# Performance work log

Measured on AMD Instinct MI355X. Metric: run time of the kernel, lower is better.

## Reference

```python
import jax, jax.numpy as jnp
import numpy as np

T, B, E, H = 512, 128, 512, 512
MEM, CTX = 500, 300

def setup_inputs() -> dict:
    key = jax.random.key(0)
    ks = jax.random.split(key, 16)
    s = 0.05
    return {
        "input_seqs": jax.random.normal(ks[0], (B, T, E), jnp.float32),
        "input_lengths": jax.random.randint(ks[1], (B,), 1, T + 1),
        "Wih_f": jax.random.normal(ks[2], (4 * H, E + CTX), jnp.float32) * s,
        "Whh_f": jax.random.normal(ks[3], (4 * H, H), jnp.float32) * s,
        "bih_f": jax.random.normal(ks[4], (4 * H,), jnp.float32) * s,
        "bhh_f": jax.random.normal(ks[5], (4 * H,), jnp.float32) * s,
        "Wih_b": jax.random.normal(ks[6], (4 * H, E + CTX), jnp.float32) * s,
        "Whh_b": jax.random.normal(ks[7], (4 * H, H), jnp.float32) * s,
        "bih_b": jax.random.normal(ks[8], (4 * H,), jnp.float32) * s,
        "bhh_b": jax.random.normal(ks[9], (4 * H,), jnp.float32) * s,
        "Mk_f": jax.random.normal(ks[10], (MEM, H), jnp.float32) * s,
        "Mv_f": jax.random.normal(ks[11], (CTX, MEM), jnp.float32) * s,
        "Mk_b": jax.random.normal(ks[12], (MEM, H), jnp.float32) * s,
        "Mv_b": jax.random.normal(ks[13], (CTX, MEM), jnp.float32) * s,
    }

def _mem_ctx(h, Mk, Mv):
    # exp-key softmax read: exp(h Mk^T) normalized by row sum, then project to CTX
    a = jnp.exp(h @ Mk.T)                      # [B, MEM]
    return (a / jnp.sum(a, axis=-1, keepdims=True)) @ Mv.T  # [B, CTX]

def _cell(x, h, c, Wih, Whh, b):
    g = x @ Wih.T + h @ Whh.T + b              # [B, 4H], gate order i,f,g,o
    i, f, gg, o = jnp.split(g, 4, axis=-1)
    c = jax.nn.sigmoid(f) * c + jax.nn.sigmoid(i) * jnp.tanh(gg)
    return jax.nn.sigmoid(o) * jnp.tanh(c), c

def reference(input_seqs, input_lengths, Wih_f, Whh_f, bih_f, bhh_f,
              Wih_b, Whh_b, bih_b, bhh_b, Mk_f, Mv_f, Mk_b, Mv_b):
    xs = jnp.transpose(input_seqs, (1, 0, 2))          # [T, B, E]
    dt = xs.dtype
    mask = (jnp.arange(T)[:, None] < input_lengths[None, :]).astype(dt)[:, :, None]  # [T,B,1]
    b_f = bih_f + bhh_f
    b_b = bih_b + bhh_b
    z = jnp.zeros((B, H), dt)
    zf = jnp.zeros((), dt)
    one = jnp.ones((), dt)

    def fstep(carry, x):
        h, c, flag = carry
        ctx = flag * _mem_ctx(h, Mk_f, Mv_f)           # step 0 uses zero dummy context
        h, c = _cell(jnp.concatenate([x, ctx], -1), h, c, Wih_f, Whh_f, b_f)
        return (h, c, one), h
    _, f_hs = jax.lax.scan(fstep, (z, z, zf), xs)      # [T, B, H] per-step hidden

    def bstep(carry, xm):
        x, m = xm
        hm, h, c, flag = carry
        ctx = flag * _mem_ctx(hm, Mk_b, Mv_b)
        h, c = _cell(jnp.concatenate([x, ctx], -1), h, c, Wih_b, Whh_b, b_b)
        return (h * m, h, c, one), None                # masked hidden feeds next memory read
    (h_b, _, _, _), _ = jax.lax.scan(bstep, (z, z, z, zf), (xs[::-1], mask[::-1]))

    idx = jnp.clip(input_lengths - 1, 0, T - 1)
    h_f = f_hs[idx, jnp.arange(B)]                     # final valid forward hidden per example
    # permute(1,2,0).view(B,-1): interleave fwd/bwd per hidden unit
    return jnp.stack([h_f, h_b], axis=-1).reshape(B, 2 * H)
```

## Files before the change

### kernel.cpp

```cpp
#include <hip/hip_runtime.h>
#include <hip/hip_bf16.h>

#define T_   512
#define B_   128
#define E_   512
#define H_   512
#define G4_  2048
#define MEM_ 500
#define CTX_ 300
#define EC_  (E_ + CTX_)

typedef short sh8  __attribute__((ext_vector_type(8)));
typedef float f32x4 __attribute__((ext_vector_type(4)));

struct ScanParams {
  const float* __restrict__ x;
  const short* __restrict__ xbf;
  const int*   __restrict__ len;
  const float* __restrict__ Wih0; const float* __restrict__ Whh0;
  const float* __restrict__ bih0; const float* __restrict__ bhh0;
  const float* __restrict__ Wih1; const float* __restrict__ Whh1;
  const float* __restrict__ bih1; const float* __restrict__ bhh1;
  const float* __restrict__ Mk0;  const float* __restrict__ Mk1;
  const float* __restrict__ Mf;
  short* __restrict__ hbf;
  short* __restrict__ hmbf;
  short* __restrict__ aB;
  unsigned* __restrict__ bar;
  float* __restrict__ out;
};

__device__ __forceinline__ float sigm_(float x) { return 1.f / (1.f + __expf(-x)); }
__device__ __forceinline__ float tanh_(float x) { return 1.f - 2.f / (__expf(2.f * x) + 1.f); }
__device__ __forceinline__ short f2bs(float f) {
  __hip_bfloat16 h = __float2bfloat16(f);
  short s; __builtin_memcpy(&s, &h, 2); return s;
}
__device__ __forceinline__ float bs2f(short s) {
  unsigned u = ((unsigned)(unsigned short)s) << 16;
  float f; __builtin_memcpy(&f, &u, 4); return f;
}

struct F16 { sh8 v[16]; };
__device__ __forceinline__ void gld16(F16& f, const short* base) {
  asm volatile(
      "global_load_dwordx4 %0, %16, off sc0 sc1\n\t"
      "global_load_dwordx4 %1, %16, off offset:64 sc0 sc1\n\t"
      "global_load_dwordx4 %2, %16, off offset:128 sc0 sc1\n\t"
      "global_load_dwordx4 %3, %16, off offset:192 sc0 sc1\n\t"
      "global_load_dwordx4 %4, %16, off offset:256 sc0 sc1\n\t"
      "global_load_dwordx4 %5, %16, off offset:320 sc0 sc1\n\t"
      "global_load_dwordx4 %6, %16, off offset:384 sc0 sc1\n\t"
      "global_load_dwordx4 %7, %16, off offset:448 sc0 sc1\n\t"
      "global_load_dwordx4 %8, %16, off offset:512 sc0 sc1\n\t"
      "global_load_dwordx4 %9, %16, off offset:576 sc0 sc1\n\t"
      "global_load_dwordx4 %10, %16, off offset:640 sc0 sc1\n\t"
      "global_load_dwordx4 %11, %16, off offset:704 sc0 sc1\n\t"
      "global_load_dwordx4 %12, %16, off offset:768 sc0 sc1\n\t"
      "global_load_dwordx4 %13, %16, off offset:832 sc0 sc1\n\t"
      "global_load_dwordx4 %14, %16, off offset:896 sc0 sc1\n\t"
      "global_load_dwordx4 %15, %16, off offset:960 sc0 sc1\n\t"
      "s_waitcnt vmcnt(0)"
      : "=&v"(f.v[0]), "=&v"(f.v[1]), "=&v"(f.v[2]), "=&v"(f.v[3]),
        "=&v"(f.v[4]), "=&v"(f.v[5]), "=&v"(f.v[6]), "=&v"(f.v[7]),
        "=&v"(f.v[8]), "=&v"(f.v[9]), "=&v"(f.v[10]), "=&v"(f.v[11]),
        "=&v"(f.v[12]), "=&v"(f.v[13]), "=&v"(f.v[14]), "=&v"(f.v[15])
      : "v"(base)
      : "memory");
}

__device__ __forceinline__ void st4s(short* base, unsigned d0, unsigned d1,
                                     unsigned d2, unsigned d3) {
  asm volatile(
      "global_store_short %4, %0, off sc0 sc1\n\t"
      "global_store_short %4, %1, off offset:1024 sc0 sc1\n\t"
      "global_store_short %4, %2, off offset:2048 sc0 sc1\n\t"
      "global_store_short %4, %3, off offset:3072 sc0 sc1\n\t"
      "s_waitcnt vmcnt(0)"
      :: "v"(d0), "v"(d1), "v"(d2), "v"(d3), "v"(base) : "memory");
}

__device__ __forceinline__ void st8s(short* base, const unsigned* d) {
  asm volatile(
      "global_store_short %8, %0, off sc0 sc1\n\t"
      "global_store_short %8, %1, off offset:1024 sc0 sc1\n\t"
      "global_store_short %8, %2, off offset:2048 sc0 sc1\n\t"
      "global_store_short %8, %3, off offset:3072 sc0 sc1\n\t"
      "global_store_short %8, %4, off offset:8 sc0 sc1\n\t"
      "global_store_short %8, %5, off offset:1032 sc0 sc1\n\t"
      "global_store_short %8, %6, off offset:2056 sc0 sc1\n\t"
      "global_store_short %8, %7, off offset:3080 sc0 sc1"
      :: "v"(d[0]), "v"(d[1]), "v"(d[2]), "v"(d[3]),
         "v"(d[4]), "v"(d[5]), "v"(d[6]), "v"(d[7]), "v"(base) : "memory");
}

__device__ __forceinline__ void bar_arrive(unsigned* slots, int w, unsigned ep) {
  __syncthreads();
  if (threadIdx.x == 0)
    __hip_atomic_store(&slots[w * 16], ep, __ATOMIC_RELAXED, __HIP_MEMORY_SCOPE_AGENT);
}
__device__ __forceinline__ void bar_wait(unsigned* slots, unsigned* rel, int w, unsigned ep) {
  if (w == 0) {
    if (threadIdx.x < 64) {
      const int l = threadIdx.x;
      for (;;) {
        unsigned a = __hip_atomic_load(&slots[l * 16], __ATOMIC_RELAXED, __HIP_MEMORY_SCOPE_AGENT);
        if (__all(a >= ep)) break;
        __builtin_amdgcn_s_sleep(1);
      }
      if (l == 0)
        __hip_atomic_store(rel, ep, __ATOMIC_RELAXED, __HIP_MEMORY_SCOPE_AGENT);
    }
    __syncthreads();
  } else {
    if (threadIdx.x == 0) {
      while (__hip_atomic_load(rel, __ATOMIC_RELAXED, __HIP_MEMORY_SCOPE_AGENT) < ep)
        __builtin_amdgcn_s_sleep(1);
    }
    __syncthreads();
  }
}

__global__ __launch_bounds__(256) void xcvt_kernel(const float* __restrict__ x,
                                                   short* __restrict__ xbf) {
  const size_t i = ((size_t)blockIdx.x * 256 + threadIdx.x) * 8;
  f32x4 a = *reinterpret_cast<const f32x4*>(x + i);
  f32x4 b = *reinterpret_cast<const f32x4*>(x + i + 4);
  sh8 v;
  #pragma unroll
  for (int j = 0; j < 4; ++j) { v[j] = f2bs(a[j]); v[4 + j] = f2bs(b[j]); }
  *reinterpret_cast<sh8*>(xbf + i) = v;
}

__global__ __launch_bounds__(256) void mfused_kernel(
    const float* __restrict__ WihF, const float* __restrict__ WihB,
    const float* __restrict__ MvF,  const float* __restrict__ MvB,
    float* __restrict__ Mf) {
  const int d  = blockIdx.x >> 7;
  const int j0 = (blockIdx.x & 127) * 16;
  const float* __restrict__ Wih = d ? WihB : WihF;
  const float* __restrict__ Mv  = d ? MvB  : MvF;
  __shared__ float Wl[16][CTX_ + 1];
  for (int i = threadIdx.x; i < 16 * CTX_; i += 256) {
    int r = i / CTX_, cc = i - r * CTX_;
    Wl[r][cc] = Wih[(size_t)(j0 + r) * EC_ + E_ + cc];
  }
  __syncthreads();
  const int jj = threadIdx.x & 15;
  for (int m = threadIdx.x >> 4; m < MEM_; m += 16) {
    float acc = 0.f;
    for (int cc = 0; cc < CTX_; ++cc)
      acc = fmaf(Mv[cc * MEM_ + m], Wl[jj][cc], acc);
    Mf[(size_t)d * MEM_ * G4_ + (size_t)m * G4_ + j0 + jj] = acc;
  }
}

__global__ __launch_bounds__(512, 1) void scan_kernel(ScanParams p) {
  const int dir  = blockIdx.x >> 6;
  const int w    = blockIdx.x & 63;
  const int tid  = threadIdx.x;
  const int wv   = tid >> 6;
  const int lane = tid & 63;

  __shared__ __align__(16) short WgL[32 * 2 * 64 * 8];
  __shared__ __align__(16) short MkL[16 * 64 * 8];
  __shared__ __align__(16) short MfL[16 * 2 * 64 * 8];
  __shared__ int LvL[B_];

  const float* __restrict__ Wihd = dir ? p.Wih1 : p.Wih0;
  const float* __restrict__ Whhd = dir ? p.Whh1 : p.Whh0;
  const float* __restrict__ bihd = dir ? p.bih1 : p.bih0;
  const float* __restrict__ bhhd = dir ? p.bhh1 : p.bhh0;
  const float* __restrict__ Mkd  = dir ? p.Mk1  : p.Mk0;
  const float* __restrict__ Mfd  = p.Mf + (size_t)dir * MEM_ * G4_;
  short* __restrict__ aBd = p.aB + (size_t)dir * B_ * 512;

  unsigned* __restrict__ slots = p.bar + dir * 2048;
  unsigned* __restrict__ rel   = p.bar + 4096 + dir * 64;

  const int ct = w >> 1;

  for (int i = tid; i < 32 * 2 * 64; i += 512) {
    const int ks = i >> 7, r2 = i & 127, ct2 = r2 >> 6, l2 = r2 & 63;
    const int col = l2 & 15, kg = l2 >> 4;
    const int k0 = ks * 32 + kg * 8;
    const int gc = (col & 3) * H_ + 8 * w + 4 * ct2 + (col >> 2);
    const float* src = (k0 < E_) ? (Wihd + (size_t)gc * EC_ + k0)
                                 : (Whhd + (size_t)gc * H_ + (k0 - E_));
    sh8 v;
    #pragma unroll
    for (int j = 0; j < 8; ++j) v[j] = f2bs(src[j]);
    *reinterpret_cast<sh8*>(&WgL[i * 8]) = v;
  }
  for (int i = tid; i < 16 * 64; i += 512) {
    const int ks = i >> 6, l2 = i & 63;
    const int col = l2 & 15, kg = l2 >> 4;
    const int k0 = ks * 32 + kg * 8;
    const int mr = 16 * ct + col;
    sh8 v;
    #pragma unroll
    for (int j = 0; j < 8; ++j)
      v[j] = (mr < MEM_) ? f2bs(Mkd[(size_t)mr * H_ + k0 + j]) : (short)0;
    *reinterpret_cast<sh8*>(&MkL[i * 8]) = v;
  }
  for (int i = tid; i < 16 * 2 * 64; i += 512) {
    const int ks = i >> 7, r2 = i & 127, ct2 = r2 >> 6, l2 = r2 & 63;
    const int col = l2 & 15, kg = l2 >> 4;
    const int gc = (col & 3) * H_ + 8 * w + 4 * ct2 + (col >> 2);
    const int m0 = ks * 32 + kg * 8;
    sh8 v;
    #pragma unroll
    for (int j = 0; j < 8; ++j)
      v[j] = (m0 + j < MEM_) ? f2bs(Mfd[(size_t)(m0 + j) * G4_ + gc]) : (short)0;
    *reinterpret_cast<sh8*>(&MfL[i * 8]) = v;
  }
  if (tid < B_) LvL[tid] = p.len[tid];

  const int cc  = lane & 15;
  const int q   = cc & 3;
  const int uu  = cc >> 2;
  const int kg8 = (lane >> 4) * 8;
  const int arow = lane & 15;
  float biasl[2];
  #pragma unroll
  for (int ct2 = 0; ct2 < 2; ++ct2) {
    const int gc = q * H_ + 8 * w + 4 * ct2 + uu;
    biasl[ct2] = bihd[gc] + bhhd[gc];
  }

  float creg[2][4] = {{0.f,0.f,0.f,0.f},{0.f,0.f,0.f,0.f}};
  __syncthreads();

  auto xhalf = [&](int t, f32x4* acc) {
    if (p.xbf) {
      const short* xb = p.xbf + ((size_t)(16 * wv + arow) * T_ + t) * E_ + kg8;
      for (int ks = 0; ks < 16; ++ks) {
        sh8 af = *reinterpret_cast<const sh8*>(xb + ks * 32);
        acc[0] = __builtin_amdgcn_mfma_f32_16x16x32_bf16(
            af, *reinterpret_cast<const sh8*>(&WgL[((ks * 2 + 0) * 64 + lane) * 8]), acc[0], 0, 0, 0);
        acc[1] = __builtin_amdgcn_mfma_f32_16x16x32_bf16(
            af, *reinterpret_cast<const sh8*>(&WgL[((ks * 2 + 1) * 64 + lane) * 8]), acc[1], 0, 0, 0);
      }
    } else {
      const float* xp0 = p.x + ((size_t)(16 * wv + arow) * T_ + t) * E_ + kg8;
      for (int ks = 0; ks < 16; ++ks) {
        f32x4 v0 = *reinterpret_cast<const f32x4*>(xp0 + ks * 32);
        f32x4 v1 = *reinterpret_cast<const f32x4*>(xp0 + ks * 32 + 4);
        sh8 af;
        #pragma unroll
        for (int j = 0; j < 4; ++j) { af[j] = f2bs(v0[j]); af[4 + j] = f2bs(v1[j]); }
        acc[0] = __builtin_amdgcn_mfma_f32_16x16x32_bf16(
            af, *reinterpret_cast<const sh8*>(&WgL[((ks * 2 + 0) * 64 + lane) * 8]), acc[0], 0, 0, 0);
        acc[1] = __builtin_amdgcn_mfma_f32_16x16x32_bf16(
            af, *reinterpret_cast<const sh8*>(&WgL[((ks * 2 + 1) * 64 + lane) * 8]), acc[1], 0, 0, 0);
      }
    }
  };

  f32x4 accG[2] = {(f32x4){0,0,0,0}, (f32x4){0,0,0,0}};
  xhalf(dir ? T_ - 1 : 0, accG);

  for (int s = 0; s < T_; ++s) {
    const int t   = dir ? (T_ - 1 - s) : s;
    const int cur = s & 1, prv = cur ^ 1;
    const short* __restrict__ hb_prev = p.hbf + ((size_t)(prv * 2 + dir)) * B_ * H_;
    short*       __restrict__ hb_cur  = p.hbf + ((size_t)(cur * 2 + dir)) * B_ * H_;
    const short* __restrict__ hm_prev = p.hmbf + (size_t)prv * B_ * H_;
    short*       __restrict__ hm_cur  = p.hmbf + (size_t)cur * B_ * H_;

    if (wv < 4) {
      const int mt = (w & 1) * 4 + wv;
      const short* __restrict__ hmem = dir ? hm_prev : hb_prev;
      F16 fA;
      gld16(fA, hmem + (size_t)(16 * mt + arow) * H_ + kg8);
      f32x4 accA = (f32x4){0, 0, 0, 0};
      for (int ks = 0; ks < 16; ++ks)
        accA = __builtin_amdgcn_mfma_f32_16x16x32_bf16(
            fA.v[ks], *reinterpret_cast<const sh8*>(&MkL[(ks * 64 + lane) * 8]), accA, 0, 0, 0);
      const int m = 16 * ct + arow;
      unsigned d[4];
      #pragma unroll
      for (int r = 0; r < 4; ++r) {
        float e = (m < MEM_) ? __expf(accA[r]) : 0.f;
        d[r] = (unsigned)(unsigned short)f2bs(e);
      }
      st4s(aBd + (size_t)(16 * mt + 4 * (lane >> 4)) * 512 + m, d[0], d[1], d[2], d[3]);
    }

    const unsigned ep1 = 2 * s + 1, ep2 = 2 * s + 2;
    bar_arrive(slots, w, ep1);

    {
      F16 fH;
      gld16(fH, hb_prev + (size_t)(16 * wv + arow) * H_ + kg8);
      for (int ks = 0; ks < 16; ++ks) {
        accG[0] = __builtin_amdgcn_mfma_f32_16x16x32_bf16(
            fH.v[ks], *reinterpret_cast<const sh8*>(&WgL[(((16 + ks) * 2 + 0) * 64 + lane) * 8]), accG[0], 0, 0, 0);
        accG[1] = __builtin_amdgcn_mfma_f32_16x16x32_bf16(
            fH.v[ks], *reinterpret_cast<const sh8*>(&WgL[(((16 + ks) * 2 + 1) * 64 + lane) * 8]), accG[1], 0, 0, 0);
      }
    }

    bar_wait(slots, rel, w, ep1);

    f32x4 accC[2] = {(f32x4){0,0,0,0}, (f32x4){0,0,0,0}};
    float rs = 0.f;
    if (s > 0) {
      F16 fC;
      gld16(fC, aBd + (size_t)(16 * wv + arow) * 512 + kg8);
      for (int ks = 0; ks < 16; ++ks) {
        accC[0] = __builtin_amdgcn_mfma_f32_16x16x32_bf16(
            fC.v[ks], *reinterpret_cast<const sh8*>(&MfL[((ks * 2 + 0) * 64 + lane) * 8]), accC[0], 0, 0, 0);
        accC[1] = __builtin_amdgcn_mfma_f32_16x16x32_bf16(
            fC.v[ks], *reinterpret_cast<const sh8*>(&MfL[((ks * 2 + 1) * 64 + lane) * 8]), accC[1], 0, 0, 0);
        #pragma unroll
        for (int j = 0; j < 8; ++j) rs += bs2f(fC.v[ks][j]);
      }
      rs += __shfl_xor(rs, 16);
      rs += __shfl_xor(rs, 32);
    }
    float inv4[4];
    #pragma unroll
    for (int r = 0; r < 4; ++r)
      inv4[r] = (s > 0) ? 1.f / __shfl(rs, 4 * (lane >> 4) + r) : 0.f;

    unsigned hsd[8]; unsigned hmd[8]; float hvv[2][4];
    #pragma unroll
    for (int ct2 = 0; ct2 < 2; ++ct2) {
      float g4[4];
      #pragma unroll
      for (int r = 0; r < 4; ++r) {
        float v = accG[ct2][r] + biasl[ct2];
        if (s > 0) v += accC[ct2][r] * inv4[r];
        g4[r] = v;
      }
      #pragma unroll
      for (int r = 0; r < 4; ++r) {
        const float x1 = __shfl_xor(g4[r], 1);
        const float x2 = __shfl_xor(g4[r], 2);
        const float x3 = __shfl_xor(g4[r], 3);
        const float iv = (q==0)?g4[r]:(q==1)?x1:(q==2)?x2:x3;
        const float fv = (q==0)?x1:(q==1)?g4[r]:(q==2)?x3:x2;
        const float gv = (q==0)?x2:(q==1)?x3:(q==2)?g4[r]:x1;
        const float ov = (q==0)?x3:(q==1)?x2:(q==2)?x1:g4[r];
        float cv = creg[ct2][r];
        cv = sigm_(fv) * cv + sigm_(iv) * tanh_(gv);
        const float hv = sigm_(ov) * tanh_(cv);
        creg[ct2][r] = cv;
        hvv[ct2][r] = hv;
        const short hs = f2bs(hv);
        hsd[ct2 * 4 + r] = (unsigned)(unsigned short)hs;
        if (dir) {
          const int b = 16 * wv + 4 * (lane >> 4) + r;
          hmd[ct2 * 4 + r] = (t < LvL[b]) ? hsd[ct2 * 4 + r] : 0u;
        }
      }
    }
    if (q == 0) {
      const int b0 = 16 * wv + 4 * (lane >> 4);
      const int unit0 = 8 * w + uu;
      unsigned hord[8] = {hsd[0],hsd[1],hsd[2],hsd[3],hsd[4],hsd[5],hsd[6],hsd[7]};
      st8s(hb_cur + (size_t)b0 * H_ + unit0, hord);
      if (dir) {
        unsigned mord[8] = {hmd[0],hmd[1],hmd[2],hmd[3],hmd[4],hmd[5],hmd[6],hmd[7]};
        st8s(hm_cur + (size_t)b0 * H_ + unit0, mord);
      }
      #pragma unroll
      for (int ct2 = 0; ct2 < 2; ++ct2) {
        #pragma unroll
        for (int r = 0; r < 4; ++r) {
          const int b = b0 + r;
          const int unit = unit0 + 4 * ct2;
          if (dir == 0) {
            if (t == LvL[b] - 1) p.out[b * (2 * H_) + 2 * unit] = hvv[ct2][r];
          } else {
            if (s == T_ - 1) p.out[b * (2 * H_) + 2 * unit + 1] = hvv[ct2][r];
          }
        }
      }
    }
    asm volatile("s_waitcnt vmcnt(0)" ::: "memory");

    bar_arrive(slots, w, ep2);

    accG[0] = (f32x4){0,0,0,0}; accG[1] = (f32x4){0,0,0,0};
    if (s + 1 < T_) xhalf(dir ? (T_ - 2 - s) : (s + 1), accG);

    bar_wait(slots, rel, w, ep2);
  }
}

extern "C" void kernel_launch(void* const* d_in, const int* in_sizes, int n_in,
                              void* d_out, int out_size, void* d_ws, size_t ws_size,
                              hipStream_t stream) {
  (void)in_sizes; (void)n_in; (void)out_size;

  ScanParams p;
  p.x    = (const float*)d_in[0];
  p.len  = (const int*)  d_in[1];
  p.Wih0 = (const float*)d_in[2];
  p.Whh0 = (const float*)d_in[3];
  p.bih0 = (const float*)d_in[4];
  p.bhh0 = (const float*)d_in[5];
  p.Wih1 = (const float*)d_in[6];
  p.Whh1 = (const float*)d_in[7];
  p.bih1 = (const float*)d_in[8];
  p.bhh1 = (const float*)d_in[9];
  p.Mk0  = (const float*)d_in[10];
  const float* MvF = (const float*)d_in[11];
  p.Mk1  = (const float*)d_in[12];
  const float* MvB = (const float*)d_in[13];

  char* ws = (char*)d_ws;
  size_t off = 0;
  auto alloc = [&](size_t bytes) -> void* {
    void* ptr = ws + off; off += (bytes + 255) & ~(size_t)255; return ptr;
  };
  float*    Mf   = (float*)   alloc((size_t)2 * MEM_ * G4_ * 4);
  short*    hbf  = (short*)   alloc((size_t)2 * 2 * B_ * H_ * 2);
  short*    hmbf = (short*)   alloc((size_t)2 * B_ * H_ * 2);
  short*    aB   = (short*)   alloc((size_t)2 * B_ * 512 * 2);
  unsigned* bar  = (unsigned*)alloc((4096 + 2 * 64) * sizeof(unsigned));
  size_t xbf_off = off;
  short*    xbf  = (short*)   alloc((size_t)B_ * T_ * E_ * 2);
  const bool useXbf = (ws_size >= xbf_off + (size_t)B_ * T_ * E_ * 2);

  p.Mf = Mf; p.hbf = hbf; p.hmbf = hmbf; p.aB = aB; p.bar = bar;
  p.xbf = useXbf ? xbf : nullptr;
  p.out = (float*)d_out;

  hipMemsetAsync(hbf, 0, (size_t)(2 * 2 + 2) * B_ * H_ * 2, stream);
  hipMemsetAsync(bar, 0, (4096 + 2 * 64) * sizeof(unsigned), stream);

  if (useXbf) {
    const size_t n8 = (size_t)B_ * T_ * E_ / 8;
    xcvt_kernel<<<dim3((unsigned)(n8 / 256)), dim3(256), 0, stream>>>(p.x, xbf);
  }
  mfused_kernel<<<dim3(256), dim3(256), 0, stream>>>(
      (const float*)d_in[2], (const float*)d_in[6], MvF, MvB, Mf);

  void* args[] = { &p };
  hipLaunchCooperativeKernel((const void*)scan_kernel, dim3(128), dim3(512),
                             args, 0, stream);
}
```

Before: 10.47 ms.

## Replace grid-wide step barriers with per-wave dataflow flags

Drops the two centralized arrive/wait grid barriers per timestep. Each wave now publishes a per-wave ready flag for its hidden-state rows and for its attention-score tile. Consumers spin only on the specific flags they depend on. The attention-score production is also reassigned: only blocks whose parity matches the direction compute it, and each wave handles its own batch rows. The aim is to cut synchronization latency on the serial recurrence critical path. In exchange there is more flag traffic, and a bounded spin that could silently proceed on a timeout.

Result: faster. 9.677 ms (-7.6%).

```diff
diff --git a/kernel.cpp b/kernel.cpp
--- a/kernel.cpp
+++ b/kernel.cpp
@@ -9,6 +9,7 @@
 #define MEM_ 500
 #define CTX_ 300
 #define EC_  (E_ + CTX_)
+#define SPIN_MAX 65536
 
 typedef short sh8  __attribute__((ext_vector_type(8)));
 typedef float f32x4 __attribute__((ext_vector_type(4)));
@@ -94,31 +95,27 @@
          "v"(d[4]), "v"(d[5]), "v"(d[6]), "v"(d[7]), "v"(base) : "memory");
 }
 
-__device__ __forceinline__ void bar_arrive(unsigned* slots, int w, unsigned ep) {
-  __syncthreads();
-  if (threadIdx.x == 0)
-    __hip_atomic_store(&slots[w * 16], ep, __ATOMIC_RELAXED, __HIP_MEMORY_SCOPE_AGENT);
-}
-__device__ __forceinline__ void bar_wait(unsigned* slots, unsigned* rel, int w, unsigned ep) {
-  if (w == 0) {
-    if (threadIdx.x < 64) {
-      const int l = threadIdx.x;
-      for (;;) {
-        unsigned a = __hip_atomic_load(&slots[l * 16], __ATOMIC_RELAXED, __HIP_MEMORY_SCOPE_AGENT);
-        if (__all(a >= ep)) break;
-        __builtin_amdgcn_s_sleep(1);
-      }
-      if (l == 0)
-        __hip_atomic_store(rel, ep, __ATOMIC_RELAXED, __HIP_MEMORY_SCOPE_AGENT);
-    }
-    __syncthreads();
-  } else {
-    if (threadIdx.x == 0) {
-      while (__hip_atomic_load(rel, __ATOMIC_RELAXED, __HIP_MEMORY_SCOPE_AGENT) < ep)
-        __builtin_amdgcn_s_sleep(1);
-    }
-    __syncthreads();
-  }
+__device__ __forceinline__ bool hchk(const unsigned* hfl, int wv, unsigned ep, int lane) {
+  unsigned v = __hip_atomic_load(&hfl[((lane * 8) + wv) * 16],
+                                 __ATOMIC_RELAXED, __HIP_MEMORY_SCOPE_AGENT);
+  return __all((int)(v >= ep));
+}
+__device__ __forceinline__ bool achk(const unsigned* afl, int wv, unsigned ep, int lane) {
+  unsigned v = __hip_atomic_load(&afl[(((lane & 31) * 8) + wv) * 16],
+                                 __ATOMIC_RELAXED, __HIP_MEMORY_SCOPE_AGENT);
+  return __all((int)(v >= ep));
+}
+__device__ __forceinline__ void spin_h(const unsigned* hfl, int wv, unsigned ep, int lane) {
+  int n = 0;
+  while (!hchk(hfl, wv, ep, lane) && n < SPIN_MAX) { __builtin_amdgcn_s_sleep(1); ++n; }
+}
+__device__ __forceinline__ void spin_a(const unsigned* afl, int wv, unsigned ep, int lane) {
+  int n = 0;
+  while (!achk(afl, wv, ep, lane) && n < SPIN_MAX) { __builtin_amdgcn_s_sleep(1); ++n; }
+}
+__device__ __forceinline__ void fset(unsigned* slot, unsigned ep, int lane) {
+  if (lane == 0)
+    __hip_atomic_store(slot, ep, __ATOMIC_RELAXED, __HIP_MEMORY_SCOPE_AGENT);
 }
 
 __global__ __launch_bounds__(256) void xcvt_kernel(const float* __restrict__ x,
@@ -175,10 +172,11 @@
   const float* __restrict__ Mfd  = p.Mf + (size_t)dir * MEM_ * G4_;
   short* __restrict__ aBd = p.aB + (size_t)dir * B_ * 512;
 
-  unsigned* __restrict__ slots = p.bar + dir * 2048;
-  unsigned* __restrict__ rel   = p.bar + 4096 + dir * 64;
-
-  const int ct = w >> 1;
+  unsigned* __restrict__ hflD = p.bar + (size_t)dir * 64 * 8 * 16;
+  unsigned* __restrict__ aflD = p.bar + 16384 + (size_t)dir * 32 * 8 * 16;
+
+  const bool prod = ((w & 1) == dir);
+  const int  ct   = w >> 1;
 
   for (int i = tid; i < 32 * 2 * 64; i += 512) {
     const int ks = i >> 7, r2 = i & 127, ct2 = r2 >> 6, l2 = r2 & 63;
@@ -260,6 +258,8 @@
   f32x4 accG[2] = {(f32x4){0,0,0,0}, (f32x4){0,0,0,0}};
   xhalf(dir ? T_ - 1 : 0, accG);
 
+  const bool bwdprod = prod && dir;
+
   for (int s = 0; s < T_; ++s) {
     const int t   = dir ? (T_ - 1 - s) : s;
     const int cur = s & 1, prv = cur ^ 1;
@@ -268,15 +268,26 @@
     const short* __restrict__ hm_prev = p.hmbf + (size_t)prv * B_ * H_;
     short*       __restrict__ hm_cur  = p.hmbf + (size_t)cur * B_ * H_;
 
-    if (wv < 4) {
-      const int mt = (w & 1) * 4 + wv;
-      const short* __restrict__ hmem = dir ? hm_prev : hb_prev;
-      F16 fA;
-      gld16(fA, hmem + (size_t)(16 * mt + arow) * H_ + kg8);
+    const short* hrow = hb_prev + (size_t)(16 * wv + arow) * H_ + kg8;
+    const short* mrow = hm_prev + (size_t)(16 * wv + arow) * H_ + kg8;
+
+    if (s > 0) spin_h(hflD, wv, (unsigned)s, lane);
+    __builtin_amdgcn_sched_barrier(0);
+    F16 fH, fM;
+    gld16(fH, hrow);
+    if (bwdprod) gld16(fM, mrow);
+
+    if (prod) {
       f32x4 accA = (f32x4){0, 0, 0, 0};
-      for (int ks = 0; ks < 16; ++ks)
-        accA = __builtin_amdgcn_mfma_f32_16x16x32_bf16(
-            fA.v[ks], *reinterpret_cast<const sh8*>(&MkL[(ks * 64 + lane) * 8]), accA, 0, 0, 0);
+      if (dir) {
+        for (int ks = 0; ks < 16; ++ks)
+          accA = __builtin_amdgcn_mfma_f32_16x16x32_bf16(
+              fM.v[ks], *reinterpret_cast<const sh8*>(&MkL[(ks * 64 + lane) * 8]), accA, 0, 0, 0);
+      } else {
+        for (int ks = 0; ks < 16; ++ks)
+          accA = __builtin_amdgcn_mfma_f32_16x16x32_bf16(
+              fH.v[ks], *reinterpret_cast<const sh8*>(&MkL[(ks * 64 + lane) * 8]), accA, 0, 0, 0);
+      }
       const int m = 16 * ct + arow;
       unsigned d[4];
       #pragma unroll
@@ -284,30 +295,25 @@
         float e = (m < MEM_) ? __expf(accA[r]) : 0.f;
         d[r] = (unsigned)(unsigned short)f2bs(e);
       }
-      st4s(aBd + (size_t)(16 * mt + 4 * (lane >> 4)) * 512 + m, d[0], d[1], d[2], d[3]);
-    }
-
-    const unsigned ep1 = 2 * s + 1, ep2 = 2 * s + 2;
-    bar_arrive(slots, w, ep1);
-
-    {
-      F16 fH;
-      gld16(fH, hb_prev + (size_t)(16 * wv + arow) * H_ + kg8);
-      for (int ks = 0; ks < 16; ++ks) {
-        accG[0] = __builtin_amdgcn_mfma_f32_16x16x32_bf16(
-            fH.v[ks], *reinterpret_cast<const sh8*>(&WgL[(((16 + ks) * 2 + 0) * 64 + lane) * 8]), accG[0], 0, 0, 0);
-        accG[1] = __builtin_amdgcn_mfma_f32_16x16x32_bf16(
-            fH.v[ks], *reinterpret_cast<const sh8*>(&WgL[(((16 + ks) * 2 + 1) * 64 + lane) * 8]), accG[1], 0, 0, 0);
-      }
-    }
-
-    bar_wait(slots, rel, w, ep1);
+      st4s(aBd + (size_t)(16 * wv + 4 * (lane >> 4)) * 512 + m, d[0], d[1], d[2], d[3]);
+      fset(&aflD[(ct * 8 + wv) * 16], (unsigned)(s + 1), lane);
+    }
+
+    for (int ks = 0; ks < 16; ++ks) {
+      accG[0] = __builtin_amdgcn_mfma_f32_16x16x32_bf16(
+          fH.v[ks], *reinterpret_cast<const sh8*>(&WgL[(((16 + ks) * 2 + 0) * 64 + lane) * 8]), accG[0], 0, 0, 0);
+      accG[1] = __builtin_amdgcn_mfma_f32_16x16x32_bf16(
+          fH.v[ks], *reinterpret_cast<const sh8*>(&WgL[(((16 + ks) * 2 + 1) * 64 + lane) * 8]), accG[1], 0, 0, 0);
+    }
 
     f32x4 accC[2] = {(f32x4){0,0,0,0}, (f32x4){0,0,0,0}};
-    float rs = 0.f;
+    float inv4[4] = {0.f, 0.f, 0.f, 0.f};
     if (s > 0) {
+      spin_a(aflD, wv, (unsigned)(s + 1), lane);
+      __builtin_amdgcn_sched_barrier(0);
       F16 fC;
       gld16(fC, aBd + (size_t)(16 * wv + arow) * 512 + kg8);
+      float rs = 0.f;
       for (int ks = 0; ks < 16; ++ks) {
         accC[0] = __builtin_amdgcn_mfma_f32_16x16x32_bf16(
             fC.v[ks], *reinterpret_cast<const sh8*>(&MfL[((ks * 2 + 0) * 64 + lane) * 8]), accC[0], 0, 0, 0);
@@ -318,11 +324,10 @@
       }
       rs += __shfl_xor(rs, 16);
       rs += __shfl_xor(rs, 32);
-    }
-    float inv4[4];
-    #pragma unroll
-    for (int r = 0; r < 4; ++r)
-      inv4[r] = (s > 0) ? 1.f / __shfl(rs, 4 * (lane >> 4) + r) : 0.f;
+      #pragma unroll
+      for (int r = 0; r < 4; ++r)
+        inv4[r] = 1.f / __shfl(rs, 4 * (lane >> 4) + r);
+    }
 
     unsigned hsd[8]; unsigned hmd[8]; float hvv[2][4];
     #pragma unroll
@@ -380,13 +385,10 @@
       }
     }
     asm volatile("s_waitcnt vmcnt(0)" ::: "memory");
-
-    bar_arrive(slots, w, ep2);
+    fset(&hflD[(w * 8 + wv) * 16], (unsigned)(s + 1), lane);
 
     accG[0] = (f32x4){0,0,0,0}; accG[1] = (f32x4){0,0,0,0};
     if (s + 1 < T_) xhalf(dir ? (T_ - 2 - s) : (s + 1), accG);
-
-    bar_wait(slots, rel, w, ep2);
   }
 }
 
@@ -420,7 +422,7 @@
   short*    hbf  = (short*)   alloc((size_t)2 * 2 * B_ * H_ * 2);
   short*    hmbf = (short*)   alloc((size_t)2 * B_ * H_ * 2);
   short*    aB   = (short*)   alloc((size_t)2 * B_ * 512 * 2);
-  unsigned* bar  = (unsigned*)alloc((4096 + 2 * 64) * sizeof(unsigned));
+  unsigned* bar  = (unsigned*)alloc((size_t)24576 * sizeof(unsigned));
   size_t xbf_off = off;
   short*    xbf  = (short*)   alloc((size_t)B_ * T_ * E_ * 2);
   const bool useXbf = (ws_size >= xbf_off + (size_t)B_ * T_ * E_ * 2);
@@ -430,7 +432,7 @@
   p.out = (float*)d_out;
 
   hipMemsetAsync(hbf, 0, (size_t)(2 * 2 + 2) * B_ * H_ * 2, stream);
-  hipMemsetAsync(bar, 0, (4096 + 2 * 64) * sizeof(unsigned), stream);
+  hipMemsetAsync(bar, 0, (size_t)24576 * sizeof(unsigned), stream);
 
   if (useXbf) {
     const size_t n8 = (size_t)B_ * T_ * E_ / 8;
```
